# Kernel optimization log

Measured on AMD Instinct MI355X. Metric: run time of the kernel, lower is better.

The kernel has to match this reference:

```python
import jax, jax.numpy as jnp
import numpy as np

B, N, D, R = 4, 2048, 1024, 64
LN_EPS = 1e-5


def setup_inputs() -> dict:
    key = jax.random.key(0)
    k_x, k_m, k_u, k_v = jax.random.split(key, 4)
    x = jax.random.normal(k_x, (B, N, D), dtype=jnp.float32)
    mask = jax.random.uniform(k_m, (B, N, R), dtype=jnp.float32)
    # xavier-style init for low-rank bases U_max, V_max: (d_model, R_max)
    scale = jnp.sqrt(2.0 / (D + R)).astype(jnp.float32)
    U = jax.random.normal(k_u, (D, R), dtype=jnp.float32) * scale
    V = jax.random.normal(k_v, (D, R), dtype=jnp.float32) * scale
    gamma = jnp.ones((D,), dtype=jnp.float32)
    beta = jnp.zeros((D,), dtype=jnp.float32)
    return {"x": x, "mask": mask, "U": U, "V": V, "gamma": gamma, "beta": beta}


def _layernorm(y, gamma, beta):
    mu = jnp.mean(y, axis=-1, keepdims=True)
    var = jnp.mean(jnp.square(y - mu), axis=-1, keepdims=True)
    return (y - mu) * jax.lax.rsqrt(var + LN_EPS) * gamma + beta


def reference(x, mask, U, V, gamma, beta):
    # Q/K: low-rank projections gated by per-token continuous mask
    Q = jnp.einsum('bnd,dr->bnr', x, U) * mask            # (B, N, R)
    K = jnp.einsum('bnd,dr->bnr', x, V) * mask            # (B, N, R)
    # effective rank per query token, clamped at 1
    r_eff = jnp.maximum(jnp.sum(mask, axis=-1, keepdims=True), 1.0)  # (B, N, 1)
    scores = jnp.einsum('bqr,bkr->bqk', Q, K) / jnp.sqrt(r_eff)      # (B, N, N)
    A = jax.nn.softmax(scores, axis=-1)
    delta = jnp.einsum('bqk,bkd->bqd', A, x)              # (B, N, D)
    # backbone is identity: out = LN(x + delta)
    return _layernorm(x + delta, gamma, beta)
```

## Files before the change

kernel.cpp:

```cpp
#include <hip/hip_runtime.h>

#define Bb 4
#define Nn 2048
#define Dd 1024
#define Rr 64
#define LN_EPS 1e-5f

typedef unsigned short u16;
typedef short bf16x8 __attribute__((ext_vector_type(8)));
typedef float f32x4 __attribute__((ext_vector_type(4)));

__device__ __forceinline__ u16 f2bf(float f) {
  unsigned u = __float_as_uint(f);
  u += 0x7FFFu + ((u >> 16) & 1u);
  return (u16)(u >> 16);
}

__device__ __forceinline__ void g2l16(u16* l, const u16* g) {
  __builtin_amdgcn_global_load_lds(
      (const __attribute__((address_space(1))) unsigned int*)g,
      (__attribute__((address_space(3))) unsigned int*)l, 16, 0, 0);
}

__global__ __launch_bounds__(256) void prep_x(const float* __restrict__ x,
                                              u16* __restrict__ xt) {
  __shared__ float tile[64][65];
  const int b = blockIdx.z;
  const int n0 = blockIdx.x * 64;
  const int d0 = blockIdx.y * 64;
  const int t = threadIdx.x;
  const int c = t & 63, r4 = t >> 6;
#pragma unroll
  for (int rr = 0; rr < 16; rr++) {
    int row = rr * 4 + r4;
    tile[row][c] = x[(size_t)(b * Nn + n0 + row) * Dd + d0 + c];
  }
  __syncthreads();
#pragma unroll
  for (int rr = 0; rr < 16; rr++) {
    int dd = rr * 4 + r4;
    xt[(size_t)(b * Dd + d0 + dd) * Nn + n0 + c] = f2bf(tile[c][dd]);
  }
}

__global__ __launch_bounds__(256) void prep_small(const float* __restrict__ U,
    const float* __restrict__ V, const float* __restrict__ mask,
    u16* __restrict__ uvt, float* __restrict__ qs) {
  if (blockIdx.x < 32) {
    __shared__ float tile[64][65];
    const int which = blockIdx.x >> 4;
    const int d0 = (blockIdx.x & 15) * 64;
    const float* src = which ? V : U;
    const int t = threadIdx.x, c = t & 63, r4 = t >> 6;
#pragma unroll
    for (int rr = 0; rr < 16; rr++) {
      int row = rr * 4 + r4;
      tile[row][c] = src[(size_t)(d0 + row) * Rr + c];
    }
    __syncthreads();
#pragma unroll
    for (int rr = 0; rr < 16; rr++) {
      int r = rr * 4 + r4;
      uvt[(size_t)(which * 64 + r) * Dd + d0 + c] = f2bf(tile[c][r]);
    }
  } else {
    const int row = (blockIdx.x - 32) * 4 + (threadIdx.x >> 6);
    const int lane = threadIdx.x & 63;
    float v = mask[(size_t)row * Rr + lane];
#pragma unroll
    for (int off = 32; off; off >>= 1) v += __shfl_xor(v, off);
    if (lane == 0) qs[row] = rsqrtf(fmaxf(v, 1.0f));
  }
}

__global__ __launch_bounds__(256) void proj_qk(const float* __restrict__ x,
    const float* __restrict__ mask, const u16* __restrict__ uvt,
    u16* __restrict__ Qo, u16* __restrict__ Ko) {
  const int t = threadIdx.x;
  const int w = t >> 6, l = t & 63, quad = l >> 4, l16 = l & 15;
  const int g0 = blockIdx.x * 32;
  f32x4 acc[2][2];
#pragma unroll
  for (int i = 0; i < 2; i++)
#pragma unroll
    for (int j = 0; j < 2; j++) acc[i][j] = (f32x4){0.f, 0.f, 0.f, 0.f};
  for (int k0 = 0; k0 < Dd; k0 += 32) {
    bf16x8 a[2];
#pragma unroll
    for (int mt = 0; mt < 2; mt++) {
      const float4* px = (const float4*)&x[(size_t)(g0 + mt * 16 + l16) * Dd + k0 + quad * 8];
      float4 x0 = px[0], x1 = px[1];
      bf16x8 av;
      av[0] = (short)f2bf(x0.x); av[1] = (short)f2bf(x0.y);
      av[2] = (short)f2bf(x0.z); av[3] = (short)f2bf(x0.w);
      av[4] = (short)f2bf(x1.x); av[5] = (short)f2bf(x1.y);
      av[6] = (short)f2bf(x1.z); av[7] = (short)f2bf(x1.w);
      a[mt] = av;
    }
    bf16x8 bfr[2];
#pragma unroll
    for (int i = 0; i < 2; i++) {
      int col = (w * 2 + i) * 16 + l16;
      bfr[i] = *(const bf16x8*)&uvt[(size_t)col * Dd + k0 + quad * 8];
    }
#pragma unroll
    for (int mt = 0; mt < 2; mt++)
#pragma unroll
      for (int i = 0; i < 2; i++)
        acc[mt][i] = __builtin_amdgcn_mfma_f32_16x16x32_bf16(a[mt], bfr[i], acc[mt][i], 0, 0, 0);
  }
#pragma unroll
  for (int mt = 0; mt < 2; mt++)
#pragma unroll
    for (int i = 0; i < 2; i++) {
      int col = (w * 2 + i) * 16 + l16;
      int r_ = col & 63;
#pragma unroll
      for (int r = 0; r < 4; r++) {
        int row = g0 + mt * 16 + quad * 4 + r;
        float v = acc[mt][i][r] * mask[(size_t)row * Rr + r_];
        u16 bv = f2bf(v);
        if (col < 64) Qo[(size_t)row * Rr + r_] = bv;
        else          Ko[(size_t)row * Rr + r_] = bv;
      }
    }
}

__global__ __launch_bounds__(512, 2) void score_softmax(
    const u16* __restrict__ Qm, const u16* __restrict__ Km,
    const float* __restrict__ qs, u16* __restrict__ Pw,
    float* __restrict__ linv_g) {
  __shared__ float red[32][8];
  __shared__ float mfin[32];
  const int t = threadIdx.x;
  const int w = t >> 6, l = t & 63, quad = l >> 4, l16 = l & 15;
  const int id = blockIdx.x;
  const int xcd = id & 7;
  const int b = xcd >> 1;
  const int q0 = (((id >> 3) << 1) | (xcd & 1)) * 32;
  bf16x8 qf[2][2];
#pragma unroll
  for (int mt = 0; mt < 2; mt++)
#pragma unroll
    for (int ks = 0; ks < 2; ks++)
      qf[mt][ks] = *(const bf16x8*)&Qm[(size_t)(b * Nn + q0 + mt * 16 + l16) * Rr + ks * 32 + quad * 8];
  f32x4 acc[2][16];
#pragma unroll
  for (int mt = 0; mt < 2; mt++)
#pragma unroll
    for (int nt = 0; nt < 16; nt++) acc[mt][nt] = (f32x4){0.f, 0.f, 0.f, 0.f};
#pragma unroll
  for (int nt = 0; nt < 16; nt++) {
#pragma unroll
    for (int ks = 0; ks < 2; ks++) {
      bf16x8 kf = *(const bf16x8*)&Km[(size_t)(b * Nn + w * 256 + nt * 16 + l16) * Rr + ks * 32 + quad * 8];
#pragma unroll
      for (int mt = 0; mt < 2; mt++)
        acc[mt][nt] = __builtin_amdgcn_mfma_f32_16x16x32_bf16(qf[mt][ks], kf, acc[mt][nt], 0, 0, 0);
    }
  }
  float sc[2][4];
#pragma unroll
  for (int mt = 0; mt < 2; mt++)
#pragma unroll
    for (int r = 0; r < 4; r++)
      sc[mt][r] = qs[(size_t)b * Nn + q0 + mt * 16 + quad * 4 + r];
#pragma unroll
  for (int mt = 0; mt < 2; mt++)
#pragma unroll
    for (int nt = 0; nt < 16; nt++)
#pragma unroll
      for (int r = 0; r < 4; r++) acc[mt][nt][r] *= sc[mt][r];
  float vmax[2][4];
#pragma unroll
  for (int mt = 0; mt < 2; mt++)
#pragma unroll
    for (int r = 0; r < 4; r++) {
      float m = -1e30f;
#pragma unroll
      for (int nt = 0; nt < 16; nt++) m = fmaxf(m, acc[mt][nt][r]);
#pragma unroll
      for (int off = 1; off < 16; off <<= 1) m = fmaxf(m, __shfl_xor(m, off));
      vmax[mt][r] = m;
    }
  if (l16 == 0) {
#pragma unroll
    for (int mt = 0; mt < 2; mt++)
#pragma unroll
      for (int r = 0; r < 4; r++) red[mt * 16 + quad * 4 + r][w] = vmax[mt][r];
  }
  __syncthreads();
  if (t < 32) {
    float m = -1e30f;
#pragma unroll
    for (int i = 0; i < 8; i++) m = fmaxf(m, red[t][i]);
    mfin[t] = m;
  }
  __syncthreads();
  float rowm[2][4], vsum[2][4];
#pragma unroll
  for (int mt = 0; mt < 2; mt++)
#pragma unroll
    for (int r = 0; r < 4; r++) {
      rowm[mt][r] = mfin[mt * 16 + quad * 4 + r];
      vsum[mt][r] = 0.f;
    }
#pragma unroll
  for (int mt = 0; mt < 2; mt++)
#pragma unroll
    for (int nt = 0; nt < 16; nt++)
#pragma unroll
      for (int r = 0; r < 4; r++) {
        float p = __expf(acc[mt][nt][r] - rowm[mt][r]);
        acc[mt][nt][r] = p;
        vsum[mt][r] += p;
      }
#pragma unroll
  for (int mt = 0; mt < 2; mt++)
#pragma unroll
    for (int r = 0; r < 4; r++) {
#pragma unroll
      for (int off = 1; off < 16; off <<= 1) vsum[mt][r] += __shfl_xor(vsum[mt][r], off);
    }
  __syncthreads();
  if (l16 == 0) {
#pragma unroll
    for (int mt = 0; mt < 2; mt++)
#pragma unroll
      for (int r = 0; r < 4; r++) red[mt * 16 + quad * 4 + r][w] = vsum[mt][r];
  }
  __syncthreads();
  if (t < 32) {
    float s = 0.f;
#pragma unroll
    for (int i = 0; i < 8; i++) s += red[t][i];
    linv_g[(size_t)b * Nn + q0 + t] = 1.f / s;
  }
#pragma unroll
  for (int mt = 0; mt < 2; mt++)
#pragma unroll
    for (int nt = 0; nt < 16; nt++) {
      const size_t base = ((size_t)(b * Nn + q0 + mt * 16 + quad * 4)) * Nn + w * 256 + nt * 16 + l16;
#pragma unroll
      for (int r = 0; r < 4; r++)
        Pw[base + (size_t)r * Nn] = f2bf(acc[mt][nt][r]);
    }
}

__global__ __launch_bounds__(256, 2) void pv_gemm(
    const u16* __restrict__ Pw, const u16* __restrict__ xt,
    const float* __restrict__ x, const float* __restrict__ linv_g,
    float* __restrict__ y) {
  __shared__ u16 As[128 * 64];
  __shared__ u16 Bs[128 * 64];
  const int t = threadIdx.x;
  const int w = t >> 6, l = t & 63, quad = l >> 4, l16 = l & 15;
  const int id = blockIdx.x;
  const int xcd = id & 7;
  const int b = xcd >> 1;
  const int nh = xcd & 1;
  const int rest = id >> 3;
  const int m0 = (rest & 15) * 128;
  const int n0 = (nh * 4 + (rest >> 4)) * 128;
  const int srow = w * 32 + (l >> 3);
  const int skoff = (((l & 7) ^ ((l >> 3) & 7)) * 8);
  f32x4 acc[4][4];
#pragma unroll
  for (int i = 0; i < 4; i++)
#pragma unroll
    for (int j = 0; j < 4; j++) acc[i][j] = (f32x4){0.f, 0.f, 0.f, 0.f};
  const int wm = w & 1, wn = w >> 1;
  const int sw = (l16 & 7);
  for (int k0 = 0; k0 < Nn; k0 += 64) {
    __syncthreads();
#pragma unroll
    for (int c = 0; c < 4; c++) {
      int row = srow + c * 8;
      g2l16(&As[(w * 32 + c * 8) * 64],
            &Pw[((size_t)(b * Nn + m0 + row)) * Nn + k0 + skoff]);
      g2l16(&Bs[(w * 32 + c * 8) * 64],
            &xt[((size_t)(b * Dd + n0 + row)) * Nn + k0 + skoff]);
    }
    __syncthreads();
#pragma unroll
    for (int ks = 0; ks < 2; ks++) {
      const int slot = ((ks * 4 + quad) ^ sw) * 8;
      bf16x8 af[4], bf_[4];
#pragma unroll
      for (int mt = 0; mt < 4; mt++)
        af[mt] = *(const bf16x8*)&As[(wm * 64 + mt * 16 + l16) * 64 + slot];
#pragma unroll
      for (int nt = 0; nt < 4; nt++)
        bf_[nt] = *(const bf16x8*)&Bs[(wn * 64 + nt * 16 + l16) * 64 + slot];
#pragma unroll
      for (int mt = 0; mt < 4; mt++)
#pragma unroll
        for (int nt = 0; nt < 4; nt++)
          acc[mt][nt] = __builtin_amdgcn_mfma_f32_16x16x32_bf16(af[mt], bf_[nt], acc[mt][nt], 0, 0, 0);
    }
  }
  float li[4][4];
#pragma unroll
  for (int mt = 0; mt < 4; mt++)
#pragma unroll
    for (int r = 0; r < 4; r++)
      li[mt][r] = linv_g[(size_t)b * Nn + m0 + wm * 64 + mt * 16 + quad * 4 + r];
#pragma unroll
  for (int mt = 0; mt < 4; mt++)
#pragma unroll
    for (int nt = 0; nt < 4; nt++) {
      const int nn = n0 + wn * 64 + nt * 16 + l16;
#pragma unroll
      for (int r = 0; r < 4; r++) {
        const int m = m0 + wm * 64 + mt * 16 + quad * 4 + r;
        const size_t off = ((size_t)(b * Nn + m)) * Dd + nn;
        y[off] = x[off] + li[mt][r] * acc[mt][nt][r];
      }
    }
}

__global__ __launch_bounds__(256) void ln_k(float* __restrict__ y,
    const float* __restrict__ gamma, const float* __restrict__ beta) {
  __shared__ float rs[4], rq[4];
  const int row = blockIdx.x;
  const int t = threadIdx.x;
  float* p = y + (size_t)row * Dd;
  float4 v = ((const float4*)p)[t];
  float s = v.x + v.y + v.z + v.w;
  float q = v.x * v.x + v.y * v.y + v.z * v.z + v.w * v.w;
#pragma unroll
  for (int off = 32; off; off >>= 1) {
    s += __shfl_xor(s, off);
    q += __shfl_xor(q, off);
  }
  if ((t & 63) == 0) { rs[t >> 6] = s; rq[t >> 6] = q; }
  __syncthreads();
  float S = rs[0] + rs[1] + rs[2] + rs[3];
  float Q2 = rq[0] + rq[1] + rq[2] + rq[3];
  float mu = S * (1.f / Dd);
  float var = Q2 * (1.f / Dd) - mu * mu;
  float rstd = rsqrtf(var + LN_EPS);
  float4 g = ((const float4*)gamma)[t];
  float4 be = ((const float4*)beta)[t];
  v.x = (v.x - mu) * rstd * g.x + be.x;
  v.y = (v.y - mu) * rstd * g.y + be.y;
  v.z = (v.z - mu) * rstd * g.z + be.z;
  v.w = (v.w - mu) * rstd * g.w + be.w;
  ((float4*)p)[t] = v;
}

extern "C" void kernel_launch(void* const* d_in, const int* in_sizes, int n_in,
                              void* d_out, int out_size, void* d_ws, size_t ws_size,
                              hipStream_t stream) {
  const float* x     = (const float*)d_in[0];
  const float* mask  = (const float*)d_in[1];
  const float* U     = (const float*)d_in[2];
  const float* V     = (const float*)d_in[3];
  const float* gamma = (const float*)d_in[4];
  const float* beta  = (const float*)d_in[5];
  float* out = (float*)d_out;
  char* ws = (char*)d_ws;
  u16*   xt   = (u16*)ws;
  u16*   Qw   = (u16*)(ws + (size_t)(16 << 20));
  u16*   Kw   = (u16*)(ws + (size_t)(17 << 20));
  u16*   uvt  = (u16*)(ws + (size_t)(18 << 20));
  float* qsb  = (float*)(ws + (size_t)(18 << 20) + (256 << 10));
  float* linv = (float*)(ws + (size_t)(18 << 20) + (288 << 10));
  u16*   Pw   = (u16*)(ws + (size_t)(19 << 20));

  prep_x       <<<dim3(Nn / 64, Dd / 64, Bb), 256, 0, stream>>>(x, xt);
  prep_small   <<<32 + (Bb * Nn) / 4, 256, 0, stream>>>(U, V, mask, uvt, qsb);
  proj_qk      <<<(Bb * Nn) / 32, 256, 0, stream>>>(x, mask, uvt, Qw, Kw);
  score_softmax<<<Bb * (Nn / 32), 512, 0, stream>>>(Qw, Kw, qsb, Pw, linv);
  pv_gemm      <<<Bb * (Nn / 128) * (Dd / 128), 256, 0, stream>>>(Pw, xt, x, linv, out);
  ln_k         <<<Bb * Nn, 256, 0, stream>>>(out, gamma, beta);
}
```

Measured before the change: 188.2 us.

## Fold rsqrt(r_eff) into Q projection and stage P stores through LDS

The per-query 1/sqrt(r_eff) scale is applied to Q in proj_qk before bf16 rounding, which removes the scale loads and multiplies from score_softmax. The P matrix write-out now goes through a per-wave LDS tile so each lane issues 16-byte row-contiguous stores instead of scattered 2-byte stores. This targets the store inefficiency of writing the large bf16 P matrix. In exchange it adds LDS usage (about 40 KB per block), which may limit occupancy, and slightly changes rounding because Q is scaled before the bf16 conversion.

```diff
diff --git a/kernel.cpp b/kernel.cpp
--- a/kernel.cpp
+++ b/kernel.cpp
@@ -75,6 +75,7 @@
 
 __global__ __launch_bounds__(256) void proj_qk(const float* __restrict__ x,
     const float* __restrict__ mask, const u16* __restrict__ uvt,
+    const float* __restrict__ qs,
     u16* __restrict__ Qo, u16* __restrict__ Ko) {
   const int t = threadIdx.x;
   const int w = t >> 6, l = t & 63, quad = l >> 4, l16 = l & 15;
@@ -119,19 +120,18 @@
       for (int r = 0; r < 4; r++) {
         int row = g0 + mt * 16 + quad * 4 + r;
         float v = acc[mt][i][r] * mask[(size_t)row * Rr + r_];
-        u16 bv = f2bf(v);
-        if (col < 64) Qo[(size_t)row * Rr + r_] = bv;
-        else          Ko[(size_t)row * Rr + r_] = bv;
+        if (col < 64) Qo[(size_t)row * Rr + r_] = f2bf(v * qs[row]);
+        else          Ko[(size_t)row * Rr + r_] = f2bf(v);
       }
     }
 }
 
 __global__ __launch_bounds__(512, 2) void score_softmax(
     const u16* __restrict__ Qm, const u16* __restrict__ Km,
-    const float* __restrict__ qs, u16* __restrict__ Pw,
-    float* __restrict__ linv_g) {
+    u16* __restrict__ Pw, float* __restrict__ linv_g) {
   __shared__ float red[32][8];
   __shared__ float mfin[32];
+  __shared__ u16 tsl[8][32][80];
   const int t = threadIdx.x;
   const int w = t >> 6, l = t & 63, quad = l >> 4, l16 = l & 15;
   const int id = blockIdx.x;
@@ -159,18 +159,6 @@
         acc[mt][nt] = __builtin_amdgcn_mfma_f32_16x16x32_bf16(qf[mt][ks], kf, acc[mt][nt], 0, 0, 0);
     }
   }
-  float sc[2][4];
-#pragma unroll
-  for (int mt = 0; mt < 2; mt++)
-#pragma unroll
-    for (int r = 0; r < 4; r++)
-      sc[mt][r] = qs[(size_t)b * Nn + q0 + mt * 16 + quad * 4 + r];
-#pragma unroll
-  for (int mt = 0; mt < 2; mt++)
-#pragma unroll
-    for (int nt = 0; nt < 16; nt++)
-#pragma unroll
-      for (int r = 0; r < 4; r++) acc[mt][nt][r] *= sc[mt][r];
   float vmax[2][4];
 #pragma unroll
   for (int mt = 0; mt < 2; mt++)
@@ -237,14 +225,24 @@
     linv_g[(size_t)b * Nn + q0 + t] = 1.f / s;
   }
 #pragma unroll
-  for (int mt = 0; mt < 2; mt++)
-#pragma unroll
-    for (int nt = 0; nt < 16; nt++) {
-      const size_t base = ((size_t)(b * Nn + q0 + mt * 16 + quad * 4)) * Nn + w * 256 + nt * 16 + l16;
-#pragma unroll
-      for (int r = 0; r < 4; r++)
-        Pw[base + (size_t)r * Nn] = f2bf(acc[mt][nt][r]);
-    }
+  for (int c = 0; c < 4; c++) {
+#pragma unroll
+    for (int mt = 0; mt < 2; mt++)
+#pragma unroll
+      for (int i = 0; i < 4; i++) {
+        const int nt = c * 4 + i;
+#pragma unroll
+        for (int r = 0; r < 4; r++)
+          tsl[w][mt * 16 + quad * 4 + r][i * 16 + l16] = f2bf(acc[mt][nt][r]);
+      }
+#pragma unroll
+    for (int it = 0; it < 4; it++) {
+      const int u = it * 64 + l;
+      const int row = u >> 3, cg = u & 7;
+      bf16x8 vv = *(const bf16x8*)&tsl[w][row][cg * 8];
+      *(bf16x8*)&Pw[((size_t)(b * Nn + q0 + row)) * Nn + w * 256 + c * 64 + cg * 8] = vv;
+    }
+  }
 }
 
 __global__ __launch_bounds__(256, 2) void pv_gemm(
@@ -370,8 +368,8 @@
 
   prep_x       <<<dim3(Nn / 64, Dd / 64, Bb), 256, 0, stream>>>(x, xt);
   prep_small   <<<32 + (Bb * Nn) / 4, 256, 0, stream>>>(U, V, mask, uvt, qsb);
-  proj_qk      <<<(Bb * Nn) / 32, 256, 0, stream>>>(x, mask, uvt, Qw, Kw);
-  score_softmax<<<Bb * (Nn / 32), 512, 0, stream>>>(Qw, Kw, qsb, Pw, linv);
+  proj_qk      <<<(Bb * Nn) / 32, 256, 0, stream>>>(x, mask, uvt, qsb, Qw, Kw);
+  score_softmax<<<Bb * (Nn / 32), 512, 0, stream>>>(Qw, Kw, Pw, linv);
   pv_gemm      <<<Bb * (Nn / 128) * (Dd / 128), 256, 0, stream>>>(Pw, xt, x, linv, out);
   ln_k         <<<Bb * Nn, 256, 0, stream>>>(out, gamma, beta);
 }
```

Result: no change. 191.8 us (+1.9%).
